# Performance work log

Measured on AMD Instinct MI355X. Metric: run time of the kernel, lower is better.

The kernel has to match this reference:

```python
import jax, jax.numpy as jnp
import numpy as np

DUNITS = 1024
ATT_DIM = 1024
EPROJ = 1024
T = 16384
SCALING = 2.0


def setup_inputs() -> dict:
    key = jax.random.key(0)
    ks = jax.random.split(key, 8)
    dec_z = jax.random.normal(ks[0], (1, DUNITS), dtype=jnp.float32)
    att_prev = jnp.zeros((1, T), dtype=jnp.float32)
    pre_compute_enc_h = jax.random.normal(ks[1], (1, T, ATT_DIM), dtype=jnp.float32)
    enc_h = jax.random.normal(ks[2], (1, T, EPROJ), dtype=jnp.float32)
    mask = jnp.zeros((1, T), dtype=jnp.float32)
    # learned params: mlp_dec Linear(dunits->att_dim), gvec Linear(att_dim->1)
    W_dec = jax.random.normal(ks[3], (DUNITS, ATT_DIM), dtype=jnp.float32) / np.sqrt(DUNITS)
    b_dec = jnp.zeros((ATT_DIM,), dtype=jnp.float32)
    w_gvec = jax.random.normal(ks[4], (ATT_DIM,), dtype=jnp.float32) / np.sqrt(ATT_DIM)
    b_gvec = jnp.zeros((), dtype=jnp.float32)
    return {
        "dec_z": dec_z,
        "att_prev": att_prev,
        "pre_compute_enc_h": pre_compute_enc_h,
        "enc_h": enc_h,
        "mask": mask,
        "W_dec": W_dec,
        "b_dec": b_dec,
        "w_gvec": w_gvec,
        "b_gvec": b_gvec,
    }


def reference(dec_z, att_prev, pre_compute_enc_h, enc_h, mask, W_dec, b_dec, w_gvec, b_gvec):
    # dec_z: [1, dunits] -> mlp_dec -> [1, 1, att_dim]
    dec_z_tiled = (dec_z @ W_dec + b_dec)[:, None, :]
    # gvec(tanh(pre + tile)).squeeze(2): [1, T]
    e = jnp.einsum("bta,a->bt", jnp.tanh(pre_compute_enc_h + dec_z_tiled), w_gvec) + b_gvec
    e = e + mask
    w = jax.nn.softmax(SCALING * e, axis=1)  # [1, T]
    c = jnp.einsum("bte,bt->be", enc_h, w)   # [1, eproj]
    return (c, w)
```

## Files before the change

### kernel.cpp

```cpp
#include <hip/hip_runtime.h>
#include <math.h>

#define TT   16384
#define ADIM 1024
#define NCH  2048
#define RPB  8
#define NCH2 64

__device__ __forceinline__ float ftanh(float x) {
    float e2 = __expf(2.0f * x);
    return 1.0f - 2.0f * __builtin_amdgcn_rcpf(e2 + 1.0f);
}

__device__ __forceinline__ float pdot(float4 p, float4 d, float4 g) {
    return ftanh(p.x + d.x) * g.x + ftanh(p.y + d.y) * g.y +
           ftanh(p.z + d.z) * g.z + ftanh(p.w + d.w) * g.w;
}

__global__ void k1_gemv_part(const float* __restrict__ z, const float* __restrict__ W,
                             float* __restrict__ part) {
    int b = blockIdx.x, tid = threadIdx.x;
    float4 acc = {0.f, 0.f, 0.f, 0.f};
#pragma unroll
    for (int i = 0; i < 4; ++i) {
        int d = b * 4 + i;
        float zv = z[d];
        float4 w4 = reinterpret_cast<const float4*>(W)[(size_t)d * 256 + tid];
        acc.x += zv * w4.x; acc.y += zv * w4.y; acc.z += zv * w4.z; acc.w += zv * w4.w;
    }
    reinterpret_cast<float4*>(part)[(size_t)b * 256 + tid] = acc;
}

__global__ void k2_gemv_red(const float* __restrict__ part, const float* __restrict__ bdec,
                            float* __restrict__ dp) {
    int b = blockIdx.x, tid = threadIdx.x;
    int lane = tid & 63, wv = tid >> 6;
    int rsub = lane >> 2;
    int colg = lane & 3;
    float4 acc = {0.f, 0.f, 0.f, 0.f};
#pragma unroll
    for (int i = 0; i < 4; ++i) {
        int row = i * 64 + wv * 16 + rsub;
        float4 v = reinterpret_cast<const float4*>(part)[(size_t)row * 256 + b * 4 + colg];
        acc.x += v.x; acc.y += v.y; acc.z += v.z; acc.w += v.w;
    }
#pragma unroll
    for (int off = 4; off <= 32; off <<= 1) {
        acc.x += __shfl_xor(acc.x, off, 64);
        acc.y += __shfl_xor(acc.y, off, 64);
        acc.z += __shfl_xor(acc.z, off, 64);
        acc.w += __shfl_xor(acc.w, off, 64);
    }
    __shared__ float4 lds[4][4];
    if (lane < 4) lds[wv][lane] = acc;
    __syncthreads();
    if (tid < 4) {
        float4 t = {0.f, 0.f, 0.f, 0.f};
#pragma unroll
        for (int w = 0; w < 4; ++w) {
            float4 v = lds[w][tid];
            t.x += v.x; t.y += v.y; t.z += v.z; t.w += v.w;
        }
        float4 bd = reinterpret_cast<const float4*>(bdec)[b * 4 + tid];
        t.x += bd.x; t.y += bd.y; t.z += bd.z; t.w += bd.w;
        reinterpret_cast<float4*>(dp)[b * 4 + tid] = t;
    }
}

#define ACC(E, PW) do { \
    ca.x += (PW) * (E).x; ca.y += (PW) * (E).y; \
    ca.z += (PW) * (E).z; ca.w += (PW) * (E).w; } while (0)

__global__ void __launch_bounds__(256) k3_fused(
    const float* __restrict__ pre, const float* __restrict__ enc,
    const float* __restrict__ dp, const float* __restrict__ wg,
    const float* __restrict__ bgp, const float* __restrict__ mask,
    float* __restrict__ e_out, float* __restrict__ m_out,
    float* __restrict__ s_out, float* __restrict__ cpart) {
    int b = blockIdx.x, tid = threadIdx.x;
    int lane = tid & 63, wv = tid >> 6;
    int col = wv * 64 + lane;
    float4 d4 = reinterpret_cast<const float4*>(dp)[col];
    float4 g4 = reinterpret_cast<const float4*>(wg)[col];
    float bgv = bgp[0];
    int t0 = b * RPB;
    const float4* pb = reinterpret_cast<const float4*>(pre) + (size_t)t0 * 256 + col;
    const float4* eb = reinterpret_cast<const float4*>(enc) + (size_t)t0 * 256 + col;

    float dt[RPB];
    {
        float4 B0 = pb[0], B1 = pb[256];
        dt[0] = pdot(B0, d4, g4); B0 = pb[512];
        dt[1] = pdot(B1, d4, g4); B1 = pb[768];
        dt[2] = pdot(B0, d4, g4); B0 = pb[1024];
        dt[3] = pdot(B1, d4, g4); B1 = pb[1280];
        dt[4] = pdot(B0, d4, g4); B0 = pb[1536];
        dt[5] = pdot(B1, d4, g4); B1 = pb[1792];
        dt[6] = pdot(B0, d4, g4);
        dt[7] = pdot(B1, d4, g4);
    }
#pragma unroll
    for (int r = 0; r < RPB; ++r) {
#pragma unroll
        for (int off = 32; off; off >>= 1) dt[r] += __shfl_xor(dt[r], off, 64);
    }
    __shared__ float sd[4][RPB];
    if (lane == 0) {
#pragma unroll
        for (int r = 0; r < RPB; ++r) sd[wv][r] = dt[r];
    }
    __syncthreads();
    float et[RPB];
#pragma unroll
    for (int r = 0; r < RPB; ++r)
        et[r] = 2.0f * (sd[0][r] + sd[1][r] + sd[2][r] + sd[3][r] + bgv + mask[t0 + r]);
    if (tid == 0) {
#pragma unroll
        for (int r = 0; r < RPB; ++r) e_out[t0 + r] = et[r];
    }

    float m = et[0];
#pragma unroll
    for (int r = 1; r < RPB; ++r) m = fmaxf(m, et[r]);
    float p[RPB], s = 0.f;
#pragma unroll
    for (int r = 0; r < RPB; ++r) { p[r] = __expf(et[r] - m); s += p[r]; }
    if (tid == 0) { m_out[b] = m; s_out[b] = s; }

    float4 ca = {0.f, 0.f, 0.f, 0.f};
    {
        float4 E0 = eb[0], E1 = eb[256];
        ACC(E0, p[0]); E0 = eb[512];
        ACC(E1, p[1]); E1 = eb[768];
        ACC(E0, p[2]); E0 = eb[1024];
        ACC(E1, p[3]); E1 = eb[1280];
        ACC(E0, p[4]); E0 = eb[1536];
        ACC(E1, p[5]); E1 = eb[1792];
        ACC(E0, p[6]);
        ACC(E1, p[7]);
    }
    reinterpret_cast<float4*>(cpart)[(size_t)b * 256 + col] = ca;
}

__global__ void __launch_bounds__(256) k4_fold(
    const float* __restrict__ m_arr, const float* __restrict__ s_arr,
    const float* __restrict__ cpart, float* __restrict__ cpart2,
    float* __restrict__ msout) {
    int b = blockIdx.x, tid = threadIdx.x;
    int lane = tid & 63, wv = tid >> 6;
    __shared__ float redm[4], reds[4];
    float mloc = -3.0e38f;
#pragma unroll
    for (int i = 0; i < NCH / 256; ++i) mloc = fmaxf(mloc, m_arr[tid + i * 256]);
#pragma unroll
    for (int off = 32; off; off >>= 1) mloc = fmaxf(mloc, __shfl_xor(mloc, off, 64));
    if (lane == 0) redm[wv] = mloc;
    __syncthreads();
    float M = fmaxf(fmaxf(redm[0], redm[1]), fmaxf(redm[2], redm[3]));
    float4 acc = {0.f, 0.f, 0.f, 0.f};
#pragma unroll
    for (int i = 0; i < NCH / NCH2; ++i) {
        int r = b * (NCH / NCH2) + i;
        float scf = __expf(m_arr[r] - M);
        float4 v = reinterpret_cast<const float4*>(cpart)[(size_t)r * 256 + tid];
        acc.x += scf * v.x; acc.y += scf * v.y; acc.z += scf * v.z; acc.w += scf * v.w;
    }
    reinterpret_cast<float4*>(cpart2)[(size_t)b * 256 + tid] = acc;
    if (b == 0) {
        float sl = 0.f;
#pragma unroll
        for (int i = 0; i < NCH / 256; ++i)
            sl += s_arr[tid + i * 256] * __expf(m_arr[tid + i * 256] - M);
#pragma unroll
        for (int off = 32; off; off >>= 1) sl += __shfl_xor(sl, off, 64);
        if (lane == 0) reds[wv] = sl;
        __syncthreads();
        if (tid == 0) {
            float S = reds[0] + reds[1] + reds[2] + reds[3];
            msout[0] = M;
            msout[1] = 1.0f / S;
        }
    }
}

__global__ void __launch_bounds__(256) k5_final(
    const float* __restrict__ cpart2, const float* __restrict__ e,
    const float* __restrict__ ms, float* __restrict__ c_out,
    float* __restrict__ w_out) {
    int b = blockIdx.x, tid = threadIdx.x;
    float M = ms[0], invS = ms[1];
    if (b < 16) {
        int rs = tid >> 4;
        int cg = tid & 15;
        float4 acc = {0.f, 0.f, 0.f, 0.f};
#pragma unroll
        for (int i = 0; i < 4; ++i) {
            int r = rs * 4 + i;
            float4 v = reinterpret_cast<const float4*>(cpart2)[(size_t)r * 256 + b * 16 + cg];
            acc.x += v.x; acc.y += v.y; acc.z += v.z; acc.w += v.w;
        }
        __shared__ float4 lds[16][16];
        lds[rs][cg] = acc;
        __syncthreads();
        if (tid < 16) {
            float4 t = {0.f, 0.f, 0.f, 0.f};
#pragma unroll
            for (int r = 0; r < 16; ++r) {
                float4 v = lds[r][tid];
                t.x += v.x; t.y += v.y; t.z += v.z; t.w += v.w;
            }
            t.x *= invS; t.y *= invS; t.z *= invS; t.w *= invS;
            reinterpret_cast<float4*>(c_out)[b * 16 + tid] = t;
        }
    } else {
        int base = (b - 16) * 256 + tid;
        float4 ev = reinterpret_cast<const float4*>(e)[base];
        float4 w;
        w.x = __expf(ev.x - M) * invS;
        w.y = __expf(ev.y - M) * invS;
        w.z = __expf(ev.z - M) * invS;
        w.w = __expf(ev.w - M) * invS;
        reinterpret_cast<float4*>(w_out)[base] = w;
    }
}

extern "C" void kernel_launch(void* const* d_in, const int* in_sizes, int n_in,
                              void* d_out, int out_size, void* d_ws, size_t ws_size,
                              hipStream_t stream) {
    const float* dec_z = (const float*)d_in[0];
    const float* pre   = (const float*)d_in[2];
    const float* enc   = (const float*)d_in[3];
    const float* mask  = (const float*)d_in[4];
    const float* W_dec = (const float*)d_in[5];
    const float* b_dec = (const float*)d_in[6];
    const float* wg    = (const float*)d_in[7];
    const float* bg    = (const float*)d_in[8];

    float* out   = (float*)d_out;
    float* c_out = out;
    float* w_out = out + ADIM;

    float* ws = (float*)d_ws;
    float* part   = ws;
    float* dp     = part + 256 * ADIM;
    float* e_sc   = dp + ADIM;
    float* m_arr  = e_sc + TT;
    float* s_arr  = m_arr + NCH;
    float* cpart  = s_arr + NCH;
    float* cpart2 = cpart + (size_t)NCH * ADIM;
    float* ms     = cpart2 + (size_t)NCH2 * ADIM;

    k1_gemv_part<<<256, 256, 0, stream>>>(dec_z, W_dec, part);
    k2_gemv_red<<<64, 256, 0, stream>>>(part, b_dec, dp);
    k3_fused<<<NCH, 256, 0, stream>>>(pre, enc, dp, wg, bg, mask,
                                      e_sc, m_arr, s_arr, cpart);
    k4_fold<<<NCH2, 256, 0, stream>>>(m_arr, s_arr, cpart, cpart2, ms);
    k5_final<<<32, 256, 0, stream>>>(cpart2, e_sc, ms, c_out, w_out);
}
```

Before: 40.11 us.

## Issue all pre and enc loads upfront in fused kernel; double fold partitions

The fused attention kernel now issues all eight pre_compute_enc_h loads and all eight enc_h loads at the start, before the tanh dot products and the softmax, instead of a two-deep rolling prefetch. The enc_h memory traffic then overlaps the score computation and the cross-wave reduction. The fold stage's partition count NCH2 goes from 64 to 128 and the final reduction loop is generalized to match. In exchange the kernel holds more live registers (16 float4 per thread), which may lower occupancy.

```diff
diff --git a/kernel.cpp b/kernel.cpp
--- a/kernel.cpp
+++ b/kernel.cpp
@@ -5,7 +5,7 @@
 #define ADIM 1024
 #define NCH  2048
 #define RPB  8
-#define NCH2 64
+#define NCH2 128
 
 __device__ __forceinline__ float ftanh(float x) {
     float e2 = __expf(2.0f * x);
@@ -66,10 +66,6 @@
         reinterpret_cast<float4*>(dp)[b * 4 + tid] = t;
     }
 }
-
-#define ACC(E, PW) do { \
-    ca.x += (PW) * (E).x; ca.y += (PW) * (E).y; \
-    ca.z += (PW) * (E).z; ca.w += (PW) * (E).w; } while (0)
 
 __global__ void __launch_bounds__(256) k3_fused(
     const float* __restrict__ pre, const float* __restrict__ enc,
@@ -87,18 +83,15 @@
     const float4* pb = reinterpret_cast<const float4*>(pre) + (size_t)t0 * 256 + col;
     const float4* eb = reinterpret_cast<const float4*>(enc) + (size_t)t0 * 256 + col;
 
+    float4 pv[RPB], ev[RPB];
+#pragma unroll
+    for (int r = 0; r < RPB; ++r) pv[r] = pb[r * 256];
+#pragma unroll
+    for (int r = 0; r < RPB; ++r) ev[r] = eb[r * 256];
+
     float dt[RPB];
-    {
-        float4 B0 = pb[0], B1 = pb[256];
-        dt[0] = pdot(B0, d4, g4); B0 = pb[512];
-        dt[1] = pdot(B1, d4, g4); B1 = pb[768];
-        dt[2] = pdot(B0, d4, g4); B0 = pb[1024];
-        dt[3] = pdot(B1, d4, g4); B1 = pb[1280];
-        dt[4] = pdot(B0, d4, g4); B0 = pb[1536];
-        dt[5] = pdot(B1, d4, g4); B1 = pb[1792];
-        dt[6] = pdot(B0, d4, g4);
-        dt[7] = pdot(B1, d4, g4);
-    }
+#pragma unroll
+    for (int r = 0; r < RPB; ++r) dt[r] = pdot(pv[r], d4, g4);
 #pragma unroll
     for (int r = 0; r < RPB; ++r) {
 #pragma unroll
@@ -128,16 +121,10 @@
     if (tid == 0) { m_out[b] = m; s_out[b] = s; }
 
     float4 ca = {0.f, 0.f, 0.f, 0.f};
-    {
-        float4 E0 = eb[0], E1 = eb[256];
-        ACC(E0, p[0]); E0 = eb[512];
-        ACC(E1, p[1]); E1 = eb[768];
-        ACC(E0, p[2]); E0 = eb[1024];
-        ACC(E1, p[3]); E1 = eb[1280];
-        ACC(E0, p[4]); E0 = eb[1536];
-        ACC(E1, p[5]); E1 = eb[1792];
-        ACC(E0, p[6]);
-        ACC(E1, p[7]);
+#pragma unroll
+    for (int r = 0; r < RPB; ++r) {
+        ca.x += p[r] * ev[r].x; ca.y += p[r] * ev[r].y;
+        ca.z += p[r] * ev[r].z; ca.w += p[r] * ev[r].w;
     }
     reinterpret_cast<float4*>(cpart)[(size_t)b * 256 + col] = ca;
 }
@@ -194,8 +181,8 @@
         int cg = tid & 15;
         float4 acc = {0.f, 0.f, 0.f, 0.f};
 #pragma unroll
-        for (int i = 0; i < 4; ++i) {
-            int r = rs * 4 + i;
+        for (int i = 0; i < NCH2 / 16; ++i) {
+            int r = rs * (NCH2 / 16) + i;
             float4 v = reinterpret_cast<const float4*>(cpart2)[(size_t)r * 256 + b * 16 + cg];
             acc.x += v.x; acc.y += v.y; acc.z += v.z; acc.w += v.w;
         }
```

After: 39.85 us. About the same (-0.6%).
